# Kernel optimization log

Hardware: AMD Instinct MI355X
Metric: run time of the kernel (lower is better)

## Reference

```python
import jax, jax.numpy as jnp
import numpy as np

EPS = 1e-05
B, I, N, O = 1024, 256, 1024, 256

def setup_inputs() -> dict:
    key = jax.random.key(0)
    ks = jax.random.split(key, 6)
    return {
        "x_re": jax.random.normal(ks[0], (B, I, 1), dtype=jnp.float32),
        "x_im": jax.random.normal(ks[1], (B, I, 1), dtype=jnp.float32),
        "G_re": jax.random.normal(ks[2], (I, N), dtype=jnp.float32) / np.sqrt(I).astype(np.float32),
        "G_im": jax.random.normal(ks[3], (I, N), dtype=jnp.float32) / np.sqrt(I).astype(np.float32),
        "s_re": jnp.ones((1, N), dtype=jnp.float32),
        "s_im": jnp.ones((1, N), dtype=jnp.float32),
        "W_re": jax.random.normal(ks[4], (N, O), dtype=jnp.float32) * np.float32(np.sqrt(5 * np.exp(2) * I / (12 * N * O))),
        "W_im": jax.random.normal(ks[5], (N, O), dtype=jnp.float32) * np.float32(np.sqrt(5 * np.exp(2) * I / (12 * N * O))),
        "b_re": jnp.zeros((1, O), dtype=jnp.float32),
        "b_im": jnp.zeros((1, O), dtype=jnp.float32),
    }

def reference(x_re, x_im, G_re, G_im, s_re, s_im, W_re, W_im, b_re, b_im):
    # (B, inputs, 1) - (inputs, neurons) -> (B, inputs, neurons); reduce over inputs
    v_re = jnp.sum((x_re - G_re) ** 2, axis=1, keepdims=True)  # (B, 1, N)
    v_im = jnp.sum((x_im - G_im) ** 2, axis=1, keepdims=True)  # (B, 1, N)
    phi_re = jnp.exp(-v_re / jnp.maximum(s_re, EPS))  # (B, 1, N)
    phi_im = jnp.exp(-v_im / jnp.maximum(s_im, EPS))  # (B, 1, N)
    # complex matmul (phi_re + i phi_im) @ (W_re + i W_im) + (b_re + i b_im)
    y_re = jnp.matmul(phi_re, W_re) - jnp.matmul(phi_im, W_im) + b_re  # (B, 1, O)
    y_im = jnp.matmul(phi_re, W_im) + jnp.matmul(phi_im, W_re) + b_im  # (B, 1, O)
    return jnp.stack([y_re, y_im], axis=-1)  # (B, 1, O, 2) = real/imag
```

## Files before the change

### kernel.cpp

```cpp
#include <hip/hip_runtime.h>
#include <math.h>

#define B_ 1024
#define I_ 256
#define N_ 1024
#define O_ 256
#define EPSV 1e-5f

typedef unsigned short u16;
typedef short bf16x8 __attribute__((ext_vector_type(8)));
typedef float f32x4 __attribute__((ext_vector_type(4)));
typedef int i32x4 __attribute__((ext_vector_type(4)));

__device__ inline u16 f2bf(float f) {
    union { float f; unsigned int u; } v; v.f = f;
    unsigned int r = v.u + 0x7FFFu + ((v.u >> 16) & 1u);
    return (u16)(r >> 16);
}


__device__ inline void transconv_frag(const float* __restrict__ in,
                                      u16* __restrict__ out, int R, int C,
                                      int r0, int c0, int t, float (*tile)[69]) {
    const int lr = t >> 2, lq = t & 3;
    #pragma unroll
    for (int j = 0; j < 4; ++j) {
        float4 v = *(const float4*)(in + (size_t)(r0 + lr) * C + c0 + lq * 16 + j * 4);
        *(float4*)&tile[lr][lq * 16 + j * 4] = v;
    }
    __syncthreads();
    const int oc = t >> 2, oq = t & 3;
    const int row = c0 + oc;
    const int ktiles = R >> 5;
    #pragma unroll
    for (int h = 0; h < 2; ++h) {
        const int k0 = r0 + oq * 16 + h * 8;
        const int kt = k0 >> 5, quad = (k0 >> 3) & 3;
        __align__(16) u16 tmp[8];
        #pragma unroll
        for (int e = 0; e < 8; ++e)
            tmp[e] = f2bf(tile[oq * 16 + h * 8 + e][oc]);
        const size_t off = ((size_t)((row >> 4) * ktiles + kt)) * 512
                         + (quad * 16 + (row & 15)) * 8;
        *(int4*)(out + off) = *(const int4*)tmp;
    }
}

__global__ __launch_bounds__(256) void prep_kernel(
    const float* __restrict__ x_re, const float* __restrict__ x_im,
    const float* __restrict__ G_re, const float* __restrict__ G_im,
    const float* __restrict__ W_re, const float* __restrict__ W_im,
    u16* __restrict__ Xfr, u16* __restrict__ Xfi,
    u16* __restrict__ GTfr, u16* __restrict__ GTfi,
    u16* __restrict__ WTfr, u16* __restrict__ WTfi,
    float* __restrict__ xsq_re, float* __restrict__ xsq_im,
    float* __restrict__ gsq_re, float* __restrict__ gsq_im)
{
    __shared__ float smem[64][69];
    const int blk = blockIdx.x, t = threadIdx.x;

    if (blk < 256) {
        const int w = t >> 6, l = t & 63;
        const int row = blk * 4 + w;
        float4 a = *((const float4*)(x_re + (size_t)row * I_) + l);
        float4 c = *((const float4*)(x_im + (size_t)row * I_) + l);
        float sr = a.x*a.x + a.y*a.y + a.z*a.z + a.w*a.w;
        float si = c.x*c.x + c.y*c.y + c.z*c.z + c.w*c.w;
        #pragma unroll
        for (int off = 32; off > 0; off >>= 1) {
            sr += __shfl_down(sr, off);
            si += __shfl_down(si, off);
        }
        if (l == 0) { xsq_re[row] = sr; xsq_im[row] = si; }
    } else if (blk < 272) {
        const int l = t & 63, w = t >> 6;
        const int n = (blk - 256) * 64 + l;
        float sr = 0.f, si = 0.f;
        for (int i = w * 64; i < w * 64 + 64; ++i) {
            float g = G_re[(size_t)i * N_ + n]; sr += g * g;
            float h = G_im[(size_t)i * N_ + n]; si += h * h;
        }
        float (*red)[64] = (float(*)[64])smem;
        red[w][l] = sr; red[4 + w][l] = si;
        __syncthreads();
        if (w == 0) {
            gsq_re[n] = red[0][l] + red[1][l] + red[2][l] + red[3][l];
            gsq_im[n] = red[4][l] + red[5][l] + red[6][l] + red[7][l];
        }
    } else if (blk < 528) {
        const int tile_lin = (blk - 272) * 4 + (t >> 6);
        const int comp = tile_lin >> 9;
        const int tl = tile_lin & 511;
        const int mt = tl >> 3, kt = tl & 7;
        const int lane = t & 63;
        const int quad = lane & 3, l16 = lane >> 2;
        const float* src = (comp ? x_im : x_re)
                         + (size_t)(mt * 16 + l16) * I_ + kt * 32 + quad * 8;
        float4 a0 = *(const float4*)src;
        float4 a1 = *(const float4*)(src + 4);
        __align__(16) u16 tmp[8];
        tmp[0] = f2bf(a0.x); tmp[1] = f2bf(a0.y); tmp[2] = f2bf(a0.z); tmp[3] = f2bf(a0.w);
        tmp[4] = f2bf(a1.x); tmp[5] = f2bf(a1.y); tmp[6] = f2bf(a1.z); tmp[7] = f2bf(a1.w);
        u16* dst = (comp ? Xfi : Xfr)
                 + (size_t)(mt * 8 + kt) * 512 + (quad * 16 + l16) * 8;
        *(int4*)dst = *(const int4*)tmp;
    } else if (blk < 656) {
        const int local = blk - 528;
        const int comp = local >> 6, rem = local & 63;
        const int rt = rem >> 4, ct = rem & 15;
        transconv_frag(comp ? G_im : G_re, comp ? GTfi : GTfr,
                       I_, N_, rt * 64, ct * 64, t, smem);
    } else {
        const int local = blk - 656;
        const int comp = local >> 6, rem = local & 63;
        const int rt = rem >> 2, ct = rem & 3;
        transconv_frag(comp ? W_im : W_re, comp ? WTfi : WTfr,
                       N_, O_, rt * 64, ct * 64, t, smem);
    }
}

__global__ __launch_bounds__(256) void phi_mfma(
    const u16* __restrict__ Xfr, const u16* __restrict__ Xfi,
    const u16* __restrict__ GTfr, const u16* __restrict__ GTfi,
    const float* __restrict__ xsq_re, const float* __restrict__ xsq_im,
    const float* __restrict__ gsq_re, const float* __restrict__ gsq_im,
    const float* __restrict__ s_re, const float* __restrict__ s_im,
    u16* __restrict__ Pfr, u16* __restrict__ Pfi)
{
    __shared__ u16 pbuf[8 * 512];
    const int z = blockIdx.z;
    const u16* Xf  = z ? Xfi : Xfr;
    const u16* GTf = z ? GTfi : GTfr;
    const float* xsq = z ? xsq_im : xsq_re;
    const float* gsq = z ? gsq_im : gsq_re;
    const float* s   = z ? s_im : s_re;
    u16* Pf = z ? Pfi : Pfr;

    const int t = threadIdx.x;
    const int w = t >> 6, lane = t & 63;
    const int quad = lane >> 4, l16 = lane & 15;
    const int mw = (w >> 1) * 32, nw = (w & 1) * 32;
    const int mt0 = blockIdx.y * 4 + (mw >> 4);
    const int nt0 = blockIdx.x * 4 + (nw >> 4);

    const u16* Ab = Xf  + lane * 8;
    const u16* Bb = GTf + lane * 8;
    const size_t a0o = (size_t)(mt0 * 8) * 512;
    const size_t a1o = (size_t)((mt0 + 1) * 8) * 512;
    const size_t b0o = (size_t)(nt0 * 8) * 512;
    const size_t b1o = (size_t)((nt0 + 1) * 8) * 512;

    bf16x8 cA0 = *(const bf16x8*)(Ab + a0o);
    bf16x8 cA1 = *(const bf16x8*)(Ab + a1o);
    bf16x8 cB0 = *(const bf16x8*)(Bb + b0o);
    bf16x8 cB1 = *(const bf16x8*)(Bb + b1o);

    f32x4 acc[2][2] = {};
    #pragma unroll
    for (int kt = 0; kt < 8; ++kt) {
        bf16x8 nA0, nA1, nB0, nB1;
        if (kt < 7) {
            const size_t ko = (size_t)(kt + 1) * 512;
            nA0 = *(const bf16x8*)(Ab + a0o + ko);
            nA1 = *(const bf16x8*)(Ab + a1o + ko);
            nB0 = *(const bf16x8*)(Bb + b0o + ko);
            nB1 = *(const bf16x8*)(Bb + b1o + ko);
        }
        acc[0][0] = __builtin_amdgcn_mfma_f32_16x16x32_bf16(cA0, cB0, acc[0][0], 0, 0, 0);
        acc[0][1] = __builtin_amdgcn_mfma_f32_16x16x32_bf16(cA0, cB1, acc[0][1], 0, 0, 0);
        acc[1][0] = __builtin_amdgcn_mfma_f32_16x16x32_bf16(cA1, cB0, acc[1][0], 0, 0, 0);
        acc[1][1] = __builtin_amdgcn_mfma_f32_16x16x32_bf16(cA1, cB1, acc[1][1], 0, 0, 0);
        cA0 = nA0; cA1 = nA1; cB0 = nB0; cB1 = nB1;
    }

    const int m0 = blockIdx.y * 64, n0 = blockIdx.x * 64;
    #pragma unroll
    for (int mt = 0; mt < 2; ++mt)
        #pragma unroll
        for (int nt = 0; nt < 2; ++nt) {
            const int col = nw + nt * 16 + l16;
            const float gq = gsq[n0 + col];
            const float inv_s = 1.0f / fmaxf(s[n0 + col], EPSV);
            #pragma unroll
            for (int r = 0; r < 4; ++r) {
                const int row = mw + mt * 16 + quad * 4 + r;
                const float v = xsq[m0 + row] - 2.0f * acc[mt][nt][r] + gq;
                const u16 p = f2bf(__expf(-v * inv_s));
                const int lt = (row >> 4) * 2 + (col >> 5);
                pbuf[lt * 512 + (((col >> 3) & 3) * 16 + (row & 15)) * 8 + (col & 7)] = p;
            }
        }
    __syncthreads();

    const int lt = t >> 5, s32 = t & 31;
    const int mt_g = blockIdx.y * 4 + (lt >> 1);
    const int kt_g = blockIdx.x * 2 + (lt & 1);
    const u16* src = pbuf + lt * 512 + s32 * 16;
    u16* dst = Pf + (size_t)(mt_g * 32 + kt_g) * 512 + s32 * 16;
    *(int4*)dst = *(const int4*)src;
    *((int4*)dst + 1) = *((const int4*)src + 1);
}

__global__ __launch_bounds__(256) void y_mfma(
    const u16* __restrict__ Pfr, const u16* __restrict__ Pfi,
    const u16* __restrict__ WTfr, const u16* __restrict__ WTfi,
    const float* __restrict__ b_re, const float* __restrict__ b_im,
    float* __restrict__ out)
{
    __shared__ float red[4][2][16][34];
    const int t = threadIdx.x;
    const int w = t >> 6, lane = t & 63;
    const int quad = lane >> 4, l16 = lane & 15;
    const int pm = blockIdx.y;
    const int wo0 = blockIdx.x * 2;

    const u16* Ar = Pfr + lane * 8;
    const u16* Ai = Pfi + lane * 8;
    const u16* Br = WTfr + lane * 8;
    const u16* Bi = WTfi + lane * 8;
    const size_t ao = (size_t)(pm * 32 + w * 8) * 512;
    const size_t b0o = (size_t)(wo0 * 32 + w * 8) * 512;
    const size_t b1o = (size_t)((wo0 + 1) * 32 + w * 8) * 512;

    bf16x8 cAr = *(const bf16x8*)(Ar + ao);
    bf16x8 cAi = *(const bf16x8*)(Ai + ao);
    bf16x8 cBr0 = *(const bf16x8*)(Br + b0o);
    bf16x8 cBi0 = *(const bf16x8*)(Bi + b0o);
    bf16x8 cBr1 = *(const bf16x8*)(Br + b1o);
    bf16x8 cBi1 = *(const bf16x8*)(Bi + b1o);

    f32x4 cr[2] = {}, ci[2] = {};
    #pragma unroll
    for (int ks = 0; ks < 8; ++ks) {
        bf16x8 nAr, nAi, nBr0, nBi0, nBr1, nBi1;
        if (ks < 7) {
            const size_t ko = (size_t)(ks + 1) * 512;
            nAr  = *(const bf16x8*)(Ar + ao + ko);
            nAi  = *(const bf16x8*)(Ai + ao + ko);
            nBr0 = *(const bf16x8*)(Br + b0o + ko);
            nBi0 = *(const bf16x8*)(Bi + b0o + ko);
            nBr1 = *(const bf16x8*)(Br + b1o + ko);
            nBi1 = *(const bf16x8*)(Bi + b1o + ko);
        }
        i32x4 tv = (*(const i32x4*)&cAi) ^ 0x80008000;
        bf16x8 cAn = *(const bf16x8*)&tv;
        cr[0] = __builtin_amdgcn_mfma_f32_16x16x32_bf16(cAr, cBr0, cr[0], 0, 0, 0);
        cr[0] = __builtin_amdgcn_mfma_f32_16x16x32_bf16(cAn, cBi0, cr[0], 0, 0, 0);
        ci[0] = __builtin_amdgcn_mfma_f32_16x16x32_bf16(cAr, cBi0, ci[0], 0, 0, 0);
        ci[0] = __builtin_amdgcn_mfma_f32_16x16x32_bf16(cAi, cBr0, ci[0], 0, 0, 0);
        cr[1] = __builtin_amdgcn_mfma_f32_16x16x32_bf16(cAr, cBr1, cr[1], 0, 0, 0);
        cr[1] = __builtin_amdgcn_mfma_f32_16x16x32_bf16(cAn, cBi1, cr[1], 0, 0, 0);
        ci[1] = __builtin_amdgcn_mfma_f32_16x16x32_bf16(cAr, cBi1, ci[1], 0, 0, 0);
        ci[1] = __builtin_amdgcn_mfma_f32_16x16x32_bf16(cAi, cBr1, ci[1], 0, 0, 0);
        cAr = nAr; cAi = nAi;
        cBr0 = nBr0; cBi0 = nBi0; cBr1 = nBr1; cBi1 = nBi1;
    }

    #pragma unroll
    for (int nt = 0; nt < 2; ++nt) {
        const int o = nt * 16 + l16;
        #pragma unroll
        for (int r = 0; r < 4; ++r) {
            const int b = quad * 4 + r;
            red[w][0][b][o] = cr[nt][r];
            red[w][1][b][o] = ci[nt][r];
        }
    }
    __syncthreads();

    const int b = t >> 4, oq = t & 15;
    const int o = oq * 2;
    const int gb = blockIdx.y * 16 + b;
    const int go = blockIdx.x * 32 + o;
    float r0 = red[0][0][b][o]   + red[1][0][b][o]   + red[2][0][b][o]   + red[3][0][b][o];
    float i0 = red[0][1][b][o]   + red[1][1][b][o]   + red[2][1][b][o]   + red[3][1][b][o];
    float r1 = red[0][0][b][o+1] + red[1][0][b][o+1] + red[2][0][b][o+1] + red[3][0][b][o+1];
    float i1 = red[0][1][b][o+1] + red[1][1][b][o+1] + red[2][1][b][o+1] + red[3][1][b][o+1];
    float4 v;
    v.x = r0 + b_re[go];     v.y = i0 + b_im[go];
    v.z = r1 + b_re[go + 1]; v.w = i1 + b_im[go + 1];
    *(float4*)(out + ((size_t)gb * O_ + go) * 2) = v;
}

extern "C" void kernel_launch(void* const* d_in, const int* in_sizes, int n_in,
                              void* d_out, int out_size, void* d_ws, size_t ws_size,
                              hipStream_t stream) {
    const float* x_re = (const float*)d_in[0];
    const float* x_im = (const float*)d_in[1];
    const float* G_re = (const float*)d_in[2];
    const float* G_im = (const float*)d_in[3];
    const float* s_re = (const float*)d_in[4];
    const float* s_im = (const float*)d_in[5];
    const float* W_re = (const float*)d_in[6];
    const float* W_im = (const float*)d_in[7];
    const float* b_re = (const float*)d_in[8];
    const float* b_im = (const float*)d_in[9];
    float* out = (float*)d_out;

    u16* Xfr  = (u16*)d_ws;
    u16* Xfi  = Xfr  + (size_t)B_ * I_;
    u16* GTfr = Xfi  + (size_t)B_ * I_;
    u16* GTfi = GTfr + (size_t)N_ * I_;
    u16* WTfr = GTfi + (size_t)N_ * I_;
    u16* WTfi = WTfr + (size_t)O_ * N_;
    u16* Pfr  = WTfi + (size_t)O_ * N_;
    u16* Pfi  = Pfr  + (size_t)B_ * N_;
    float* xsq_re = (float*)(Pfi + (size_t)B_ * N_);
    float* xsq_im = xsq_re + B_;
    float* gsq_re = xsq_im + B_;
    float* gsq_im = gsq_re + N_;

    prep_kernel<<<784, 256, 0, stream>>>(
        x_re, x_im, G_re, G_im, W_re, W_im,
        Xfr, Xfi, GTfr, GTfi, WTfr, WTfi,
        xsq_re, xsq_im, gsq_re, gsq_im);

    phi_mfma<<<dim3(N_ / 64, B_ / 64, 2), 256, 0, stream>>>(
        Xfr, Xfi, GTfr, GTfi, xsq_re, xsq_im, gsq_re, gsq_im,
        s_re, s_im, Pfr, Pfi);

    y_mfma<<<dim3(O_ / 32, B_ / 16), 256, 0, stream>>>(
        Pfr, Pfi, WTfr, WTfi, b_re, b_im, out);
}
```

Baseline: 95.75 us.

## Fuse prep conversion into phi GEMM kernel, staging bf16 tiles in LDS

Merges the prep kernel and the phi MFMA kernel into one launch. Each block now loads its fp32 x and G tiles, converts them to bf16 fragment layout in shared memory, and computes the row and column squared norms locally, then runs the MFMA and exp epilogue. W transposition runs in extra blocks of the same launch. This removes one launch and the global round trip of the bf16 X/G copies and norms. In exchange, x and G are re-read and re-converted by every block that needs them, and the kernel uses about 73KB of LDS, which limits occupancy.

```diff
diff --git a/kernel.cpp b/kernel.cpp
--- a/kernel.cpp
+++ b/kernel.cpp
@@ -46,145 +46,132 @@
     }
 }
 
-__global__ __launch_bounds__(256) void prep_kernel(
+__global__ __launch_bounds__(256) void phiW_kernel(
     const float* __restrict__ x_re, const float* __restrict__ x_im,
     const float* __restrict__ G_re, const float* __restrict__ G_im,
     const float* __restrict__ W_re, const float* __restrict__ W_im,
-    u16* __restrict__ Xfr, u16* __restrict__ Xfi,
-    u16* __restrict__ GTfr, u16* __restrict__ GTfi,
+    const float* __restrict__ s_re, const float* __restrict__ s_im,
     u16* __restrict__ WTfr, u16* __restrict__ WTfi,
-    float* __restrict__ xsq_re, float* __restrict__ xsq_im,
-    float* __restrict__ gsq_re, float* __restrict__ gsq_im)
+    u16* __restrict__ Pfr, u16* __restrict__ Pfi)
 {
-    __shared__ float smem[64][69];
+    __shared__ __align__(16) char shraw[74880];
     const int blk = blockIdx.x, t = threadIdx.x;
 
-    if (blk < 256) {
-        const int w = t >> 6, l = t & 63;
-        const int row = blk * 4 + w;
-        float4 a = *((const float4*)(x_re + (size_t)row * I_) + l);
-        float4 c = *((const float4*)(x_im + (size_t)row * I_) + l);
-        float sr = a.x*a.x + a.y*a.y + a.z*a.z + a.w*a.w;
-        float si = c.x*c.x + c.y*c.y + c.z*c.z + c.w*c.w;
-        #pragma unroll
-        for (int off = 32; off > 0; off >>= 1) {
-            sr += __shfl_down(sr, off);
-            si += __shfl_down(si, off);
-        }
-        if (l == 0) { xsq_re[row] = sr; xsq_im[row] = si; }
-    } else if (blk < 272) {
-        const int l = t & 63, w = t >> 6;
-        const int n = (blk - 256) * 64 + l;
-        float sr = 0.f, si = 0.f;
-        for (int i = w * 64; i < w * 64 + 64; ++i) {
-            float g = G_re[(size_t)i * N_ + n]; sr += g * g;
-            float h = G_im[(size_t)i * N_ + n]; si += h * h;
-        }
-        float (*red)[64] = (float(*)[64])smem;
-        red[w][l] = sr; red[4 + w][l] = si;
-        __syncthreads();
-        if (w == 0) {
-            gsq_re[n] = red[0][l] + red[1][l] + red[2][l] + red[3][l];
-            gsq_im[n] = red[4][l] + red[5][l] + red[6][l] + red[7][l];
-        }
-    } else if (blk < 528) {
-        const int tile_lin = (blk - 272) * 4 + (t >> 6);
-        const int comp = tile_lin >> 9;
-        const int tl = tile_lin & 511;
-        const int mt = tl >> 3, kt = tl & 7;
-        const int lane = t & 63;
-        const int quad = lane & 3, l16 = lane >> 2;
-        const float* src = (comp ? x_im : x_re)
-                         + (size_t)(mt * 16 + l16) * I_ + kt * 32 + quad * 8;
-        float4 a0 = *(const float4*)src;
-        float4 a1 = *(const float4*)(src + 4);
-        __align__(16) u16 tmp[8];
-        tmp[0] = f2bf(a0.x); tmp[1] = f2bf(a0.y); tmp[2] = f2bf(a0.z); tmp[3] = f2bf(a0.w);
-        tmp[4] = f2bf(a1.x); tmp[5] = f2bf(a1.y); tmp[6] = f2bf(a1.z); tmp[7] = f2bf(a1.w);
-        u16* dst = (comp ? Xfi : Xfr)
-                 + (size_t)(mt * 8 + kt) * 512 + (quad * 16 + l16) * 8;
-        *(int4*)dst = *(const int4*)tmp;
-    } else if (blk < 656) {
-        const int local = blk - 528;
-        const int comp = local >> 6, rem = local & 63;
-        const int rt = rem >> 4, ct = rem & 15;
-        transconv_frag(comp ? G_im : G_re, comp ? GTfi : GTfr,
-                       I_, N_, rt * 64, ct * 64, t, smem);
-    } else {
-        const int local = blk - 656;
+    if (blk >= 512) {
+        const int local = blk - 512;
         const int comp = local >> 6, rem = local & 63;
         const int rt = rem >> 2, ct = rem & 3;
         transconv_frag(comp ? W_im : W_re, comp ? WTfi : WTfr,
-                       N_, O_, rt * 64, ct * 64, t, smem);
-    }
-}
-
-__global__ __launch_bounds__(256) void phi_mfma(
-    const u16* __restrict__ Xfr, const u16* __restrict__ Xfi,
-    const u16* __restrict__ GTfr, const u16* __restrict__ GTfi,
-    const float* __restrict__ xsq_re, const float* __restrict__ xsq_im,
-    const float* __restrict__ gsq_re, const float* __restrict__ gsq_im,
-    const float* __restrict__ s_re, const float* __restrict__ s_im,
-    u16* __restrict__ Pfr, u16* __restrict__ Pfi)
-{
-    __shared__ u16 pbuf[8 * 512];
-    const int z = blockIdx.z;
-    const u16* Xf  = z ? Xfi : Xfr;
-    const u16* GTf = z ? GTfi : GTfr;
-    const float* xsq = z ? xsq_im : xsq_re;
-    const float* gsq = z ? gsq_im : gsq_re;
-    const float* s   = z ? s_im : s_re;
+                       N_, O_, rt * 64, ct * 64, t, (float(*)[69])shraw);
+        return;
+    }
+
+    u16*   Af    = (u16*)shraw;
+    u16*   Bf    = (u16*)(shraw + 32768);
+    float (*slab)[69] = (float(*)[69])(shraw + 65536);
+    float* xsq_l = (float*)(shraw + 65536 + 8832);
+    float* gsq_l = xsq_l + 64;
+    u16*   pbuf  = (u16*)(shraw + 65536);
+
+    const int z = blk >> 8, rem = blk & 255;
+    const int by = rem >> 4, bx = rem & 15;
+    const float* Xsrc = z ? x_im : x_re;
+    const float* Gsrc = z ? G_im : G_re;
+    const float* s    = z ? s_im : s_re;
     u16* Pf = z ? Pfi : Pfr;
-
-    const int t = threadIdx.x;
+    const int m0 = by * 64, n0 = bx * 64;
+
+    {
+        const int lr = t >> 2, lq = t & 3;
+        const float* xrow = Xsrc + (size_t)(m0 + lr) * I_;
+        float xs = 0.f;
+        #pragma unroll
+        for (int jj = 0; jj < 4; ++jj) {
+            const int k0 = jj * 64 + lq * 16;
+            float4 v0 = *(const float4*)(xrow + k0);
+            float4 v1 = *(const float4*)(xrow + k0 + 4);
+            float4 v2 = *(const float4*)(xrow + k0 + 8);
+            float4 v3 = *(const float4*)(xrow + k0 + 12);
+            xs += v0.x*v0.x + v0.y*v0.y + v0.z*v0.z + v0.w*v0.w
+                + v1.x*v1.x + v1.y*v1.y + v1.z*v1.z + v1.w*v1.w
+                + v2.x*v2.x + v2.y*v2.y + v2.z*v2.z + v2.w*v2.w
+                + v3.x*v3.x + v3.y*v3.y + v3.z*v3.z + v3.w*v3.w;
+            __align__(16) u16 c0[8], c1[8];
+            c0[0]=f2bf(v0.x); c0[1]=f2bf(v0.y); c0[2]=f2bf(v0.z); c0[3]=f2bf(v0.w);
+            c0[4]=f2bf(v1.x); c0[5]=f2bf(v1.y); c0[6]=f2bf(v1.z); c0[7]=f2bf(v1.w);
+            c1[0]=f2bf(v2.x); c1[1]=f2bf(v2.y); c1[2]=f2bf(v2.z); c1[3]=f2bf(v2.w);
+            c1[4]=f2bf(v3.x); c1[5]=f2bf(v3.y); c1[6]=f2bf(v3.z); c1[7]=f2bf(v3.w);
+            const int kt = k0 >> 5, quad = (k0 >> 3) & 3;
+            u16* tb = Af + ((size_t)((lr >> 4) * 8 + kt)) * 512;
+            *(int4*)(tb + (quad * 16 + (lr & 15)) * 8)       = *(const int4*)c0;
+            *(int4*)(tb + ((quad + 1) * 16 + (lr & 15)) * 8) = *(const int4*)c1;
+        }
+        xs += __shfl_xor(xs, 1);
+        xs += __shfl_xor(xs, 2);
+        if (lq == 0) xsq_l[lr] = xs;
+    }
+
+    {
+        const int r32 = t >> 3, seg = t & 7;
+        const int oc = t >> 2, oq = t & 3;
+        float gs = 0.f;
+        for (int sl = 0; sl < 8; ++sl) {
+            const float* grow = Gsrc + (size_t)(sl * 32 + r32) * N_ + n0 + seg * 8;
+            float4 g0 = *(const float4*)grow;
+            float4 g1 = *(const float4*)(grow + 4);
+            __syncthreads();
+            *(float4*)&slab[r32][seg * 8]     = g0;
+            *(float4*)&slab[r32][seg * 8 + 4] = g1;
+            __syncthreads();
+            __align__(16) u16 tmp[8];
+            #pragma unroll
+            for (int e = 0; e < 8; ++e) {
+                const float g = slab[oq * 8 + e][oc];
+                gs += g * g;
+                tmp[e] = f2bf(g);
+            }
+            u16* tb = Bf + ((size_t)((oc >> 4) * 8 + sl)) * 512;
+            *(int4*)(tb + (oq * 16 + (oc & 15)) * 8) = *(const int4*)tmp;
+        }
+        gs += __shfl_xor(gs, 1);
+        gs += __shfl_xor(gs, 2);
+        if (oq == 0) gsq_l[oc] = gs;
+        __syncthreads();
+    }
+
     const int w = t >> 6, lane = t & 63;
     const int quad = lane >> 4, l16 = lane & 15;
+    const int mtl = (w >> 1) * 2, ntl = (w & 1) * 2;
     const int mw = (w >> 1) * 32, nw = (w & 1) * 32;
-    const int mt0 = blockIdx.y * 4 + (mw >> 4);
-    const int nt0 = blockIdx.x * 4 + (nw >> 4);
-
-    const u16* Ab = Xf  + lane * 8;
-    const u16* Bb = GTf + lane * 8;
-    const size_t a0o = (size_t)(mt0 * 8) * 512;
-    const size_t a1o = (size_t)((mt0 + 1) * 8) * 512;
-    const size_t b0o = (size_t)(nt0 * 8) * 512;
-    const size_t b1o = (size_t)((nt0 + 1) * 8) * 512;
-
-    bf16x8 cA0 = *(const bf16x8*)(Ab + a0o);
-    bf16x8 cA1 = *(const bf16x8*)(Ab + a1o);
-    bf16x8 cB0 = *(const bf16x8*)(Bb + b0o);
-    bf16x8 cB1 = *(const bf16x8*)(Bb + b1o);
+    const u16* Abase = Af + lane * 8;
+    const u16* Bbase = Bf + lane * 8;
 
     f32x4 acc[2][2] = {};
     #pragma unroll
     for (int kt = 0; kt < 8; ++kt) {
-        bf16x8 nA0, nA1, nB0, nB1;
-        if (kt < 7) {
-            const size_t ko = (size_t)(kt + 1) * 512;
-            nA0 = *(const bf16x8*)(Ab + a0o + ko);
-            nA1 = *(const bf16x8*)(Ab + a1o + ko);
-            nB0 = *(const bf16x8*)(Bb + b0o + ko);
-            nB1 = *(const bf16x8*)(Bb + b1o + ko);
-        }
-        acc[0][0] = __builtin_amdgcn_mfma_f32_16x16x32_bf16(cA0, cB0, acc[0][0], 0, 0, 0);
-        acc[0][1] = __builtin_amdgcn_mfma_f32_16x16x32_bf16(cA0, cB1, acc[0][1], 0, 0, 0);
-        acc[1][0] = __builtin_amdgcn_mfma_f32_16x16x32_bf16(cA1, cB0, acc[1][0], 0, 0, 0);
-        acc[1][1] = __builtin_amdgcn_mfma_f32_16x16x32_bf16(cA1, cB1, acc[1][1], 0, 0, 0);
-        cA0 = nA0; cA1 = nA1; cB0 = nB0; cB1 = nB1;
-    }
-
-    const int m0 = blockIdx.y * 64, n0 = blockIdx.x * 64;
+        bf16x8 a0 = *(const bf16x8*)(Abase + (size_t)(mtl * 8 + kt) * 512);
+        bf16x8 a1 = *(const bf16x8*)(Abase + (size_t)((mtl + 1) * 8 + kt) * 512);
+        bf16x8 b0 = *(const bf16x8*)(Bbase + (size_t)(ntl * 8 + kt) * 512);
+        bf16x8 b1 = *(const bf16x8*)(Bbase + (size_t)((ntl + 1) * 8 + kt) * 512);
+        acc[0][0] = __builtin_amdgcn_mfma_f32_16x16x32_bf16(a0, b0, acc[0][0], 0, 0, 0);
+        acc[0][1] = __builtin_amdgcn_mfma_f32_16x16x32_bf16(a0, b1, acc[0][1], 0, 0, 0);
+        acc[1][0] = __builtin_amdgcn_mfma_f32_16x16x32_bf16(a1, b0, acc[1][0], 0, 0, 0);
+        acc[1][1] = __builtin_amdgcn_mfma_f32_16x16x32_bf16(a1, b1, acc[1][1], 0, 0, 0);
+    }
+
+    __syncthreads();
+
     #pragma unroll
     for (int mt = 0; mt < 2; ++mt)
         #pragma unroll
         for (int nt = 0; nt < 2; ++nt) {
             const int col = nw + nt * 16 + l16;
-            const float gq = gsq[n0 + col];
+            const float gq = gsq_l[col];
             const float inv_s = 1.0f / fmaxf(s[n0 + col], EPSV);
             #pragma unroll
             for (int r = 0; r < 4; ++r) {
                 const int row = mw + mt * 16 + quad * 4 + r;
-                const float v = xsq[m0 + row] - 2.0f * acc[mt][nt][r] + gq;
+                const float v = xsq_l[row] - 2.0f * acc[mt][nt][r] + gq;
                 const u16 p = f2bf(__expf(-v * inv_s));
                 const int lt = (row >> 4) * 2 + (col >> 5);
                 pbuf[lt * 512 + (((col >> 3) & 3) * 16 + (row & 15)) * 8 + (col & 7)] = p;
@@ -193,8 +180,8 @@
     __syncthreads();
 
     const int lt = t >> 5, s32 = t & 31;
-    const int mt_g = blockIdx.y * 4 + (lt >> 1);
-    const int kt_g = blockIdx.x * 2 + (lt & 1);
+    const int mt_g = by * 4 + (lt >> 1);
+    const int kt_g = bx * 2 + (lt & 1);
     const u16* src = pbuf + lt * 512 + s32 * 16;
     u16* dst = Pf + (size_t)(mt_g * 32 + kt_g) * 512 + s32 * 16;
     *(int4*)dst = *(const int4*)src;
@@ -297,27 +284,14 @@
     const float* b_im = (const float*)d_in[9];
     float* out = (float*)d_out;
 
-    u16* Xfr  = (u16*)d_ws;
-    u16* Xfi  = Xfr  + (size_t)B_ * I_;
-    u16* GTfr = Xfi  + (size_t)B_ * I_;
-    u16* GTfi = GTfr + (size_t)N_ * I_;
-    u16* WTfr = GTfi + (size_t)N_ * I_;
+    u16* WTfr = (u16*)d_ws;
     u16* WTfi = WTfr + (size_t)O_ * N_;
     u16* Pfr  = WTfi + (size_t)O_ * N_;
     u16* Pfi  = Pfr  + (size_t)B_ * N_;
-    float* xsq_re = (float*)(Pfi + (size_t)B_ * N_);
-    float* xsq_im = xsq_re + B_;
-    float* gsq_re = xsq_im + B_;
-    float* gsq_im = gsq_re + N_;
-
-    prep_kernel<<<784, 256, 0, stream>>>(
-        x_re, x_im, G_re, G_im, W_re, W_im,
-        Xfr, Xfi, GTfr, GTfi, WTfr, WTfi,
-        xsq_re, xsq_im, gsq_re, gsq_im);
-
-    phi_mfma<<<dim3(N_ / 64, B_ / 64, 2), 256, 0, stream>>>(
-        Xfr, Xfi, GTfr, GTfi, xsq_re, xsq_im, gsq_re, gsq_im,
-        s_re, s_im, Pfr, Pfi);
+
+    phiW_kernel<<<640, 256, 0, stream>>>(
+        x_re, x_im, G_re, G_im, W_re, W_im, s_re, s_im,
+        WTfr, WTfi, Pfr, Pfi);
 
     y_mfma<<<dim3(O_ / 32, B_ / 16), 256, 0, stream>>>(
         Pfr, Pfi, WTfr, WTfi, b_re, b_im, out);
```

New measurement: 93.67 us. 1.02x faster.
